# Optimization experiments

Hardware: AMD Instinct MI355X
Metric: run time of the kernel (lower is better)

Reference implementation:

```python
import jax, jax.numpy as jnp
import numpy as np

N, K, F, W = 32768, 32, 4, 256

def setup_inputs() -> dict:
    key = jax.random.key(0)
    ks = jax.random.split(key, 12)
    init = lambda k, shape, fan_in: jax.random.normal(k, shape, jnp.float32) / np.sqrt(fan_in)
    return {
        "h_center": jax.random.normal(ks[0], (N, W), jnp.float32),
        "h_neighbors": jax.random.normal(ks[1], (N, K, W), jnp.float32),
        "differences": jax.random.normal(ks[2], (N, K, F), jnp.float32),
        # filter MLP (depth=2): Dense(W) -> silu -> Dense(W)
        "W_f1": init(ks[3], (F, W), F),
        "b_f1": jnp.zeros((W,), jnp.float32),
        "W_f2": init(ks[4], (W, W), W),
        "b_f2": jnp.zeros((W,), jnp.float32),
        # neighbor projection Dense(W)
        "W_nb": init(ks[5], (W, W), W),
        "b_nb": jnp.zeros((W,), jnp.float32),
        # center projection Dense(W)
        "W_c": init(ks[6], (W, W), W),
        "b_c": jnp.zeros((W,), jnp.float32),
    }

def reference(h_center, h_neighbors, differences, W_f1, b_f1, W_f2, b_f2, W_nb, b_nb, W_c, b_c):
    # filter MLP over edge (difference) features: [N,K,F] -> [N,K,W]
    f = jax.nn.silu(differences @ W_f1 + b_f1)
    filter_kernel = f @ W_f2 + b_f2
    # project neighbor features: [N,K,W]
    h_nb = h_neighbors @ W_nb + b_nb
    # gated message, sum over neighbor axis -> [N,W]
    msg = jnp.sum(filter_kernel * h_nb, axis=-2)
    # center dense + message, silu
    h_out = jax.nn.silu(h_center @ W_c + b_c + msg)
    return h_out
```

## Files before the change

### kernel.cpp

```cpp
#include <hip/hip_runtime.h>
#include <hip/hip_bf16.h>
#include <stdint.h>

#define NN 32768
#define KNBR 32

typedef __attribute__((ext_vector_type(8))) short short8;
typedef __attribute__((ext_vector_type(4))) float f32x4;

__device__ __forceinline__ unsigned int f2bf(float x) {
    union { float f; unsigned int u; } c; c.f = x;
    return (c.u + 0x7FFFu + ((c.u >> 16) & 1u)) >> 16;
}
__device__ __forceinline__ unsigned int pk2(float a, float b) {
    return f2bf(a) | (f2bf(b) << 16);
}
__device__ __forceinline__ unsigned int pkr(float a, float b) {
    unsigned ua = __float_as_uint(a) + 0x8000u;
    unsigned ub = __float_as_uint(b) + 0x8000u;
    return (ua >> 16) | (ub & 0xFFFF0000u);
}
__device__ __forceinline__ float bflo(unsigned u) { return __uint_as_float(u << 16); }
__device__ __forceinline__ float bfhi(unsigned u) { return __uint_as_float(u & 0xFFFF0000u); }
__device__ __forceinline__ float silu_f(float x) {
    return x / (1.0f + __expf(-x));
}

__global__ void prep_weights(const float* __restrict__ Wf2,
                             const float* __restrict__ Wnb,
                             const float* __restrict__ Wc,
                             uint4* __restrict__ ws_out) {
    int t = blockIdx.x * 256 + threadIdx.x;
    int w = t >> 13;
    int q = t & 8191;
    int kt = q >> 10;
    int nt = (q >> 6) & 15;
    int lane = q & 63;
    int k0 = kt * 32 + ((lane >> 4) << 3);
    int col = nt * 16 + (lane & 15);
    const float* src = (w == 0) ? Wf2 : (w == 1) ? Wnb : Wc;
    const float* p = src + (size_t)k0 * 256 + col;
    uint4 o;
    o.x = pk2(p[0],        p[256]);
    o.y = pk2(p[512],      p[768]);
    o.z = pk2(p[1024],     p[1280]);
    o.w = pk2(p[1536],     p[1792]);
    ws_out[t] = o;
}

__global__ __launch_bounds__(1024, 4) void msg_kernel(
        const float* __restrict__ nbr,
        const float* __restrict__ diff,
        const float* __restrict__ Wf1,
        const float* __restrict__ b1,
        const float* __restrict__ b2,
        const float* __restrict__ bnb,
        const uint4* __restrict__ wf2_g,
        const uint4* __restrict__ wnb_g,
        float* __restrict__ msg_out)
{
    __shared__ uint4 w2l[4096];
    __shared__ uint4 wnl[4096];
    __shared__ uint4 fbuf[512];
    __shared__ uint4 ebuf[512];
    __shared__ unsigned w1p[640];

    const int tid  = threadIdx.x;
    const int lane = tid & 63;
    const int wid  = tid >> 6;
    const int wm   = wid >> 2;
    const int wn   = wid & 3;
    const int xcd  = blockIdx.x & 7;
    const int yy   = blockIdx.x >> 3;
    const int chalf = yy & 1;
    const int rgrp  = xcd * 32 + (yy >> 1);
    const size_t rowbase = (size_t)rgrp * 4096;
    const int colbase = chalf * 128;

    const int srow = tid >> 3;
    const int kq4  = (tid & 7) * 4;
    const int kq2  = (tid & 7) * 2;
    unsigned long long* const fdst = (unsigned long long*)
        ((char*)&fbuf[(srow >> 4) * 64 + (kq4 >> 3) * 16 + (srow & 15)] + ((kq4 >> 2) & 1) * 8);
    unsigned long long* const edst = (unsigned long long*)
        ((char*)&ebuf[(srow >> 4) * 64 + (kq4 >> 3) * 16 + (srow & 15)] + ((kq4 >> 2) & 1) * 8);

    auto eload = [&](int g) -> float4 {
        return *(const float4*)(nbr + (rowbase + (size_t)(g >> 3) * 128 + srow) * 256
                                + (g & 7) * 32 + kq4);
    };
    auto dload = [&](int tt) -> float4 {
        return *(const float4*)(diff + (rowbase + (size_t)tt * 128 + srow) * 4);
    };
    auto ewrite = [&](float4 v) {
        unsigned lo = pkr(v.x, v.y), hi = pkr(v.z, v.w);
        *edst = ((unsigned long long)hi << 32) | lo;
    };
    auto fstage = [&](int ktn, float4 d) {
        unsigned ov[2];
        #pragma unroll
        for (int pp = 0; pp < 2; ++pp) {
            const int ci = ktn * 16 + kq2 + pp;
            unsigned c0 = w1p[ci], c1 = w1p[128 + ci], c2 = w1p[256 + ci],
                     c3 = w1p[384 + ci], cb = w1p[512 + ci];
            float pA = bflo(cb) + d.x * bflo(c0) + d.y * bflo(c1)
                                + d.z * bflo(c2) + d.w * bflo(c3);
            float pB = bfhi(cb) + d.x * bfhi(c0) + d.y * bfhi(c1)
                                + d.z * bfhi(c2) + d.w * bfhi(c3);
            ov[pp] = pkr(silu_f(pA), silu_f(pB));
        }
        *fdst = ((unsigned long long)ov[1] << 32) | ov[0];
    };

    #pragma unroll
    for (int i = 0; i < 4; ++i) {
        int idx = tid + i * 1024;
        int kt = idx >> 9, rem = idx & 511;
        int src = kt * 1024 + chalf * 512 + rem;
        w2l[idx] = wf2_g[src];
        wnl[idx] = wnb_g[src];
    }
    if (tid < 512) {
        int j = tid >> 7, p = tid & 127;
        w1p[tid] = pk2(Wf1[j * 256 + 2 * p], Wf1[j * 256 + 2 * p + 1]);
    } else if (tid < 640) {
        int p = tid - 512;
        w1p[tid] = pk2(b1[2 * p], b1[2 * p + 1]);
    }
    float4 d4 = dload(0);
    float4 Ecur = eload(0);
    float vb2[2], vbn[2];
    #pragma unroll
    for (int n = 0; n < 2; ++n) {
        const int col = colbase + wn * 32 + n * 16 + (lane & 15);
        vb2[n] = b2[col];
        vbn[n] = bnb[col];
    }
    __syncthreads();

    ewrite(Ecur);
    fstage(0, d4);
    float4 Enext = eload(1);
    asm volatile("s_waitcnt lgkmcnt(0)" ::: "memory");
    __builtin_amdgcn_sched_barrier(0);
    __builtin_amdgcn_s_barrier();

    f32x4 accP[2][2], accH[2][2];
    #pragma unroll
    for (int m = 0; m < 2; ++m)
        #pragma unroll
        for (int n = 0; n < 2; ++n) {
            accP[m][n] = (f32x4){0.f, 0.f, 0.f, 0.f};
            accH[m][n] = (f32x4){0.f, 0.f, 0.f, 0.f};
        }

    const short8* fb8 = (const short8*)fbuf;
    const short8* eb8 = (const short8*)ebuf;
    const short8* w28 = (const short8*)w2l;
    const short8* wn8 = (const short8*)wnl;

    for (int t = 0; t < 32; ++t) {
        float4 d4n = d4;
        #pragma unroll
        for (int kt = 0; kt < 8; ++kt) {
            const int g = t * 8 + kt;
            if (kt == 0 && t + 1 < 32) d4n = dload(t + 1);
            float4 Efar = Enext;
            if (g + 2 < 256) Efar = eload(g + 2);
            short8 aF0 = fb8[(wm * 2 + 0) * 64 + lane];
            short8 aF1 = fb8[(wm * 2 + 1) * 64 + lane];
            short8 aE0 = eb8[(wm * 2 + 0) * 64 + lane];
            short8 aE1 = eb8[(wm * 2 + 1) * 64 + lane];
            asm volatile("s_waitcnt lgkmcnt(0)" ::: "memory");
            __builtin_amdgcn_sched_barrier(0);
            __builtin_amdgcn_s_barrier();
            short8 B20 = w28[(kt * 8 + wn * 2 + 0) * 64 + lane];
            short8 B21 = w28[(kt * 8 + wn * 2 + 1) * 64 + lane];
            short8 Bn0 = wn8[(kt * 8 + wn * 2 + 0) * 64 + lane];
            short8 Bn1 = wn8[(kt * 8 + wn * 2 + 1) * 64 + lane];
            accP[0][0] = __builtin_amdgcn_mfma_f32_16x16x32_bf16(aF0, B20, accP[0][0], 0, 0, 0);
            accP[0][1] = __builtin_amdgcn_mfma_f32_16x16x32_bf16(aF0, B21, accP[0][1], 0, 0, 0);
            accP[1][0] = __builtin_amdgcn_mfma_f32_16x16x32_bf16(aF1, B20, accP[1][0], 0, 0, 0);
            accP[1][1] = __builtin_amdgcn_mfma_f32_16x16x32_bf16(aF1, B21, accP[1][1], 0, 0, 0);
            accH[0][0] = __builtin_amdgcn_mfma_f32_16x16x32_bf16(aE0, Bn0, accH[0][0], 0, 0, 0);
            accH[0][1] = __builtin_amdgcn_mfma_f32_16x16x32_bf16(aE0, Bn1, accH[0][1], 0, 0, 0);
            accH[1][0] = __builtin_amdgcn_mfma_f32_16x16x32_bf16(aE1, Bn0, accH[1][0], 0, 0, 0);
            accH[1][1] = __builtin_amdgcn_mfma_f32_16x16x32_bf16(aE1, Bn1, accH[1][1], 0, 0, 0);
            if (g + 1 < 256) {
                ewrite(Enext);
                fstage((kt + 1) & 7, (kt == 7) ? d4n : d4);
            }
            if (kt == 7) {
                const size_t node = (size_t)rgrp * 128 + t * 4 + wm;
                #pragma unroll
                for (int n = 0; n < 2; ++n) {
                    float s = 0.f;
                    #pragma unroll
                    for (int m = 0; m < 2; ++m)
                        #pragma unroll
                        for (int r = 0; r < 4; ++r)
                            s += (accP[m][n][r] + vb2[n]) * (accH[m][n][r] + vbn[n]);
                    s += __shfl_xor(s, 16);
                    s += __shfl_xor(s, 32);
                    if (lane < 16)
                        msg_out[node * 256 + colbase + wn * 32 + n * 16 + lane] = s;
                }
                #pragma unroll
                for (int m = 0; m < 2; ++m)
                    #pragma unroll
                    for (int n = 0; n < 2; ++n) {
                        accP[m][n] = (f32x4){0.f, 0.f, 0.f, 0.f};
                        accH[m][n] = (f32x4){0.f, 0.f, 0.f, 0.f};
                    }
            }
            asm volatile("s_waitcnt lgkmcnt(0)" ::: "memory");
            __builtin_amdgcn_sched_barrier(0);
            __builtin_amdgcn_s_barrier();
            Enext = Efar;
        }
        d4 = d4n;
    }
}

__global__ __launch_bounds__(256) void out_kernel(
        const float* __restrict__ hc,
        const float* __restrict__ bc,
        const uint4* __restrict__ wc_g,
        float* __restrict__ out)
{
    __shared__ unsigned short a_s[4 * 2 * 64 * 8];
    __shared__ unsigned short wc_s[2 * 16 * 64 * 8];

    const int tid  = threadIdx.x;
    const int lane = tid & 63;
    const int wn   = tid >> 6;
    const int rblk = blockIdx.x * 64;

    f32x4 acc[4][4];
    #pragma unroll
    for (int mt = 0; mt < 4; ++mt)
        #pragma unroll
        for (int nt = 0; nt < 4; ++nt)
            acc[mt][nt] = (f32x4){0.f, 0.f, 0.f, 0.f};

    uint4* af4 = (uint4*)a_s;
    for (int kt2 = 0; kt2 < 4; ++kt2) {
        {
            int row = tid >> 2, quarter = tid & 3;
            const float* src = hc + (size_t)(rblk + row) * 256 + kt2 * 64 + quarter * 16;
            float4 v0 = *(const float4*)(src + 0);
            float4 v1 = *(const float4*)(src + 4);
            float4 v2 = *(const float4*)(src + 8);
            float4 v3 = *(const float4*)(src + 12);
            uint4 p0, p1;
            p0.x = pk2(v0.x, v0.y); p0.y = pk2(v0.z, v0.w);
            p0.z = pk2(v1.x, v1.y); p0.w = pk2(v1.z, v1.w);
            p1.x = pk2(v2.x, v2.y); p1.y = pk2(v2.z, v2.w);
            p1.z = pk2(v3.x, v3.y); p1.w = pk2(v3.z, v3.w);
            int mt = row >> 4, kti = quarter >> 1, fr = row & 15;
            int g0 = (quarter & 1) * 2;
            af4[(mt * 2 + kti) * 64 + g0 * 16 + fr]       = p0;
            af4[(mt * 2 + kti) * 64 + (g0 + 1) * 16 + fr] = p1;
            const uint4* srcw = wc_g + kt2 * 2048;
            uint4* dw = (uint4*)wc_s;
            #pragma unroll
            for (int j = 0; j < 8; ++j)
                dw[j * 256 + tid] = srcw[j * 256 + tid];
        }
        __syncthreads();
        #pragma unroll
        for (int kti = 0; kti < 2; ++kti) {
            short8 b[4];
            #pragma unroll
            for (int nt = 0; nt < 4; ++nt)
                b[nt] = *(const short8*)&wc_s[((kti * 16 + wn * 4 + nt) * 64 + lane) * 8];
            #pragma unroll
            for (int mt = 0; mt < 4; ++mt) {
                short8 a = *(const short8*)&a_s[((mt * 2 + kti) * 64 + lane) * 8];
                #pragma unroll
                for (int nt = 0; nt < 4; ++nt)
                    acc[mt][nt] = __builtin_amdgcn_mfma_f32_16x16x32_bf16(a, b[nt], acc[mt][nt], 0, 0, 0);
            }
        }
        __syncthreads();
    }

    #pragma unroll
    for (int mt = 0; mt < 4; ++mt)
        #pragma unroll
        for (int nt = 0; nt < 4; ++nt)
            #pragma unroll
            for (int r = 0; r < 4; ++r) {
                int grow = rblk + mt * 16 + ((lane >> 4) << 2) + r;
                int col  = wn * 64 + nt * 16 + (lane & 15);
                size_t idx = (size_t)grow * 256 + col;
                float v = acc[mt][nt][r] + bc[col] + out[idx];
                out[idx] = silu_f(v);
            }
}

extern "C" void kernel_launch(void* const* d_in, const int* in_sizes, int n_in,
                              void* d_out, int out_size, void* d_ws, size_t ws_size,
                              hipStream_t stream) {
    const float* h_center    = (const float*)d_in[0];
    const float* h_neighbors = (const float*)d_in[1];
    const float* differences = (const float*)d_in[2];
    const float* W_f1        = (const float*)d_in[3];
    const float* b_f1        = (const float*)d_in[4];
    const float* W_f2        = (const float*)d_in[5];
    const float* b_f2        = (const float*)d_in[6];
    const float* W_nb        = (const float*)d_in[7];
    const float* b_nb        = (const float*)d_in[8];
    const float* W_c         = (const float*)d_in[9];
    const float* b_c         = (const float*)d_in[10];
    float* out = (float*)d_out;

    uint4* ws4 = (uint4*)d_ws;
    const uint4* wf2_ws = ws4;
    const uint4* wnb_ws = ws4 + 8192;
    const uint4* wc_ws  = ws4 + 16384;

    prep_weights<<<96, 256, 0, stream>>>(W_f2, W_nb, W_c, ws4);
    msg_kernel<<<512, 1024, 0, stream>>>(
        h_neighbors, differences, W_f1, b_f1, b_f2, b_nb, wf2_ws, wnb_ws, out);
    out_kernel<<<NN / 64, 256, 0, stream>>>(h_center, b_c, wc_ws, out);
}
```

Measured before the change: 726.9 us.

## Specialize staging threads for filter and neighbor tiles with swizzled LDS layout

Splits the staging work so the upper 512 threads load and convert neighbor rows as 16-byte chunks, while groups of 128 lower threads each own one k-slice of the filter MLP. Those groups keep their Wf1 and bias coefficients in fp32 registers, which removes the LDS table and its bf16 unpacking. The filter and neighbor buffers now use an XOR-swizzled layout with 16-byte stores, and MFMA fragment reads use a matching permuted lane index, to cut bank conflicts. The cost is load imbalance: the filter work now lands on one 128-thread group per step, and register pressure rises under the 1024-thread launch bound.

```diff
diff --git a/kernel.cpp b/kernel.cpp
--- a/kernel.cpp
+++ b/kernel.cpp
@@ -20,8 +20,6 @@
     unsigned ub = __float_as_uint(b) + 0x8000u;
     return (ua >> 16) | (ub & 0xFFFF0000u);
 }
-__device__ __forceinline__ float bflo(unsigned u) { return __uint_as_float(u << 16); }
-__device__ __forceinline__ float bfhi(unsigned u) { return __uint_as_float(u & 0xFFFF0000u); }
 __device__ __forceinline__ float silu_f(float x) {
     return x / (1.0f + __expf(-x));
 }
@@ -63,7 +61,6 @@
     __shared__ uint4 wnl[4096];
     __shared__ uint4 fbuf[512];
     __shared__ uint4 ebuf[512];
-    __shared__ unsigned w1p[640];
 
     const int tid  = threadIdx.x;
     const int lane = tid & 63;
@@ -77,39 +74,79 @@
     const size_t rowbase = (size_t)rgrp * 4096;
     const int colbase = chalf * 128;
 
-    const int srow = tid >> 3;
-    const int kq4  = (tid & 7) * 4;
-    const int kq2  = (tid & 7) * 2;
-    unsigned long long* const fdst = (unsigned long long*)
-        ((char*)&fbuf[(srow >> 4) * 64 + (kq4 >> 3) * 16 + (srow & 15)] + ((kq4 >> 2) & 1) * 8);
-    unsigned long long* const edst = (unsigned long long*)
-        ((char*)&ebuf[(srow >> 4) * 64 + (kq4 >> 3) * 16 + (srow & 15)] + ((kq4 >> 2) & 1) * 8);
-
-    auto eload = [&](int g) -> float4 {
-        return *(const float4*)(nbr + (rowbase + (size_t)(g >> 3) * 128 + srow) * 256
-                                + (g & 7) * 32 + kq4);
+    const int fo   = tid >> 5;
+    const int fcoh = tid >> 7;
+    const int foq  = fo & 3;
+    const int frr  = tid & 31;
+    const int fidx0 = ((frr >> 4) * 64) + foq * 16 + ((frr & 15) ^ (foq << 2));
+
+    const bool isE = (tid >= 512);
+    const int et   = tid & 511;
+    const int erow = et >> 2, eq = et & 3;
+    const int eidx = ((erow >> 4) * 64) + eq * 16 + ((erow & 15) ^ (eq << 2));
+
+    const int lx = lane ^ ((lane >> 4) << 2);
+
+    float cw[4][8], cb[8];
+    {
+        const int kb = fo * 8;
+        #pragma unroll
+        for (int j = 0; j < 4; ++j) {
+            float4 a = *(const float4*)(Wf1 + j * 256 + kb);
+            float4 b = *(const float4*)(Wf1 + j * 256 + kb + 4);
+            cw[j][0]=a.x; cw[j][1]=a.y; cw[j][2]=a.z; cw[j][3]=a.w;
+            cw[j][4]=b.x; cw[j][5]=b.y; cw[j][6]=b.z; cw[j][7]=b.w;
+        }
+        float4 a = *(const float4*)(b1 + kb);
+        float4 b = *(const float4*)(b1 + kb + 4);
+        cb[0]=a.x; cb[1]=a.y; cb[2]=a.z; cb[3]=a.w;
+        cb[4]=b.x; cb[5]=b.y; cb[6]=b.z; cb[7]=b.w;
+    }
+    float vb2[2], vbn[2];
+    #pragma unroll
+    for (int n = 0; n < 2; ++n) {
+        const int col = colbase + wn * 32 + n * 16 + (lane & 15);
+        vb2[n] = b2[col];
+        vbn[n] = bnb[col];
+    }
+
+    float4 d4r[4];
+    float4 EnA, EnB, EfA, EfB;
+
+    auto dissue = [&](int s) {
+        const size_t rb = rowbase + (size_t)(s >> 3) * 128;
+        #pragma unroll
+        for (int m = 0; m < 4; ++m)
+            d4r[m] = *(const float4*)(diff + (rb + frr + 32 * m) * 4);
     };
-    auto dload = [&](int tt) -> float4 {
-        return *(const float4*)(diff + (rowbase + (size_t)tt * 128 + srow) * 4);
+    auto fstage = [&]() {
+        #pragma unroll
+        for (int m = 0; m < 4; ++m) {
+            const float4 d = d4r[m];
+            unsigned ov[4];
+            #pragma unroll
+            for (int p = 0; p < 4; ++p) {
+                float pA = cb[2*p]   + d.x*cw[0][2*p]   + d.y*cw[1][2*p]
+                                     + d.z*cw[2][2*p]   + d.w*cw[3][2*p];
+                float pB = cb[2*p+1] + d.x*cw[0][2*p+1] + d.y*cw[1][2*p+1]
+                                     + d.z*cw[2][2*p+1] + d.w*cw[3][2*p+1];
+                ov[p] = pkr(silu_f(pA), silu_f(pB));
+            }
+            uint4 o4; o4.x = ov[0]; o4.y = ov[1]; o4.z = ov[2]; o4.w = ov[3];
+            fbuf[fidx0 + m * 128] = o4;
+        }
     };
-    auto ewrite = [&](float4 v) {
-        unsigned lo = pkr(v.x, v.y), hi = pkr(v.z, v.w);
-        *edst = ((unsigned long long)hi << 32) | lo;
+    auto eload = [&](int s, float4& ea, float4& eb) {
+        const float* p = nbr + (rowbase + (size_t)(s >> 3) * 128 + erow) * 256
+                         + (s & 7) * 32 + eq * 8;
+        ea = *(const float4*)p;
+        eb = *(const float4*)(p + 4);
     };
-    auto fstage = [&](int ktn, float4 d) {
-        unsigned ov[2];
-        #pragma unroll
-        for (int pp = 0; pp < 2; ++pp) {
-            const int ci = ktn * 16 + kq2 + pp;
-            unsigned c0 = w1p[ci], c1 = w1p[128 + ci], c2 = w1p[256 + ci],
-                     c3 = w1p[384 + ci], cb = w1p[512 + ci];
-            float pA = bflo(cb) + d.x * bflo(c0) + d.y * bflo(c1)
-                                + d.z * bflo(c2) + d.w * bflo(c3);
-            float pB = bfhi(cb) + d.x * bfhi(c0) + d.y * bfhi(c1)
-                                + d.z * bfhi(c2) + d.w * bfhi(c3);
-            ov[pp] = pkr(silu_f(pA), silu_f(pB));
-        }
-        *fdst = ((unsigned long long)ov[1] << 32) | ov[0];
+    auto ewrite = [&](const float4& ea, const float4& eb) {
+        uint4 o;
+        o.x = pkr(ea.x, ea.y); o.y = pkr(ea.z, ea.w);
+        o.z = pkr(eb.x, eb.y); o.w = pkr(eb.z, eb.w);
+        ebuf[eidx] = o;
     };
 
     #pragma unroll
@@ -120,30 +157,11 @@
         w2l[idx] = wf2_g[src];
         wnl[idx] = wnb_g[src];
     }
-    if (tid < 512) {
-        int j = tid >> 7, p = tid & 127;
-        w1p[tid] = pk2(Wf1[j * 256 + 2 * p], Wf1[j * 256 + 2 * p + 1]);
-    } else if (tid < 640) {
-        int p = tid - 512;
-        w1p[tid] = pk2(b1[2 * p], b1[2 * p + 1]);
-    }
-    float4 d4 = dload(0);
-    float4 Ecur = eload(0);
-    float vb2[2], vbn[2];
-    #pragma unroll
-    for (int n = 0; n < 2; ++n) {
-        const int col = colbase + wn * 32 + n * 16 + (lane & 15);
-        vb2[n] = b2[col];
-        vbn[n] = bnb[col];
-    }
+    if (isE) { float4 a, b; eload(0, a, b); ewrite(a, b); }
+    if (fcoh == 0) { dissue(0); fstage(); }
     __syncthreads();
-
-    ewrite(Ecur);
-    fstage(0, d4);
-    float4 Enext = eload(1);
-    asm volatile("s_waitcnt lgkmcnt(0)" ::: "memory");
-    __builtin_amdgcn_sched_barrier(0);
-    __builtin_amdgcn_s_barrier();
+    if (isE) eload(1, EnA, EnB);
+    if (fcoh == 1) dissue(1);
 
     f32x4 accP[2][2], accH[2][2];
     #pragma unroll
@@ -160,17 +178,19 @@
     const short8* wn8 = (const short8*)wnl;
 
     for (int t = 0; t < 32; ++t) {
-        float4 d4n = d4;
         #pragma unroll
         for (int kt = 0; kt < 8; ++kt) {
             const int g = t * 8 + kt;
-            if (kt == 0 && t + 1 < 32) d4n = dload(t + 1);
-            float4 Efar = Enext;
-            if (g + 2 < 256) Efar = eload(g + 2);
-            short8 aF0 = fb8[(wm * 2 + 0) * 64 + lane];
-            short8 aF1 = fb8[(wm * 2 + 1) * 64 + lane];
-            short8 aE0 = eb8[(wm * 2 + 0) * 64 + lane];
-            short8 aE1 = eb8[(wm * 2 + 1) * 64 + lane];
+            if (g + 2 < 256) {
+                if (isE) eload(g + 2, EfA, EfB);
+                if (((kt + 2) & 7) == fcoh && (g + 2) >> 3 == (g + 2) / 8)
+                    ;
+                if (((g + 2) & 7) == fcoh) dissue(g + 2);
+            }
+            short8 aF0 = fb8[(wm * 2 + 0) * 64 + lx];
+            short8 aF1 = fb8[(wm * 2 + 1) * 64 + lx];
+            short8 aE0 = eb8[(wm * 2 + 0) * 64 + lx];
+            short8 aE1 = eb8[(wm * 2 + 1) * 64 + lx];
             asm volatile("s_waitcnt lgkmcnt(0)" ::: "memory");
             __builtin_amdgcn_sched_barrier(0);
             __builtin_amdgcn_s_barrier();
@@ -187,8 +207,8 @@
             accH[1][0] = __builtin_amdgcn_mfma_f32_16x16x32_bf16(aE1, Bn0, accH[1][0], 0, 0, 0);
             accH[1][1] = __builtin_amdgcn_mfma_f32_16x16x32_bf16(aE1, Bn1, accH[1][1], 0, 0, 0);
             if (g + 1 < 256) {
-                ewrite(Enext);
-                fstage((kt + 1) & 7, (kt == 7) ? d4n : d4);
+                if (isE) ewrite(EnA, EnB);
+                if (((g + 1) & 7) == fcoh) fstage();
             }
             if (kt == 7) {
                 const size_t node = (size_t)rgrp * 128 + t * 4 + wm;
@@ -216,9 +236,8 @@
             asm volatile("s_waitcnt lgkmcnt(0)" ::: "memory");
             __builtin_amdgcn_sched_barrier(0);
             __builtin_amdgcn_s_barrier();
-            Enext = Efar;
-        }
-        d4 = d4n;
+            EnA = EfA; EnB = EfB;
+        }
     }
 }
 
```

New measurement: 1.748 ms. +140.5%, slower.

## Precompute filter-MLP first layer into global bf16 fragments; double-buffer neighbor tile

Applied to the files above, without the earlier changes.

Moves silu(differences@W_f1+b_f1) out of the main message kernel into a separate prep_f kernel. That kernel writes the result as bf16 MFMA A-fragments to workspace, and msg_kernel reads them directly from global with one step of register prefetch. The neighbor LDS buffer becomes double-buffered, which removes one of the two block barriers per k-step. The intent is to take the per-step VALU/exp work and a barrier off the MFMA loop. In exchange it adds roughly a 512MB intermediate that is written once and read by both column halves, and it relies on the workspace being large enough.

```diff
diff --git a/kernel.cpp b/kernel.cpp
--- a/kernel.cpp
+++ b/kernel.cpp
@@ -20,8 +20,6 @@
     unsigned ub = __float_as_uint(b) + 0x8000u;
     return (ua >> 16) | (ub & 0xFFFF0000u);
 }
-__device__ __forceinline__ float bflo(unsigned u) { return __uint_as_float(u << 16); }
-__device__ __forceinline__ float bfhi(unsigned u) { return __uint_as_float(u & 0xFFFF0000u); }
 __device__ __forceinline__ float silu_f(float x) {
     return x / (1.0f + __expf(-x));
 }
@@ -48,22 +46,64 @@
     ws_out[t] = o;
 }
 
-__global__ __launch_bounds__(1024, 4) void msg_kernel(
-        const float* __restrict__ nbr,
+__global__ __launch_bounds__(256) void prep_f(
         const float* __restrict__ diff,
         const float* __restrict__ Wf1,
         const float* __restrict__ b1,
+        uint4* __restrict__ fout)
+{
+    const int bid  = blockIdx.x;
+    const int kt   = bid & 7;
+    const size_t g128 = (size_t)(bid >> 3);
+    const int tid  = threadIdx.x;
+    const int lane = tid & 63;
+    const int wv   = tid >> 6;
+    const int kgrp = lane >> 4, r16 = lane & 15;
+    const int k0   = kt * 32 + kgrp * 8;
+
+    float4 cwa[4], cwb[4];
+    #pragma unroll
+    for (int j = 0; j < 4; ++j) {
+        cwa[j] = *(const float4*)(Wf1 + j * 256 + k0);
+        cwb[j] = *(const float4*)(Wf1 + j * 256 + k0 + 4);
+    }
+    const float4 cba = *(const float4*)(b1 + k0);
+    const float4 cbb = *(const float4*)(b1 + k0 + 4);
+
+    #pragma unroll
+    for (int mi = 0; mi < 2; ++mi) {
+        const int mt = mi * 4 + wv;
+        const size_t row = g128 * 128 + mt * 16 + r16;
+        const float4 d = *(const float4*)(diff + row * 4);
+        float v0 = cba.x + d.x*cwa[0].x + d.y*cwa[1].x + d.z*cwa[2].x + d.w*cwa[3].x;
+        float v1 = cba.y + d.x*cwa[0].y + d.y*cwa[1].y + d.z*cwa[2].y + d.w*cwa[3].y;
+        float v2 = cba.z + d.x*cwa[0].z + d.y*cwa[1].z + d.z*cwa[2].z + d.w*cwa[3].z;
+        float v3 = cba.w + d.x*cwa[0].w + d.y*cwa[1].w + d.z*cwa[2].w + d.w*cwa[3].w;
+        float v4 = cbb.x + d.x*cwb[0].x + d.y*cwb[1].x + d.z*cwb[2].x + d.w*cwb[3].x;
+        float v5 = cbb.y + d.x*cwb[0].y + d.y*cwb[1].y + d.z*cwb[2].y + d.w*cwb[3].y;
+        float v6 = cbb.z + d.x*cwb[0].z + d.y*cwb[1].z + d.z*cwb[2].z + d.w*cwb[3].z;
+        float v7 = cbb.w + d.x*cwb[0].w + d.y*cwb[1].w + d.z*cwb[2].w + d.w*cwb[3].w;
+        uint4 o;
+        o.x = pkr(silu_f(v0), silu_f(v1));
+        o.y = pkr(silu_f(v2), silu_f(v3));
+        o.z = pkr(silu_f(v4), silu_f(v5));
+        o.w = pkr(silu_f(v6), silu_f(v7));
+        fout[(size_t)bid * 512 + mt * 64 + lane] = o;
+    }
+}
+
+__global__ __launch_bounds__(1024, 4) void msg_kernel(
+        const float* __restrict__ nbr,
         const float* __restrict__ b2,
         const float* __restrict__ bnb,
         const uint4* __restrict__ wf2_g,
         const uint4* __restrict__ wnb_g,
+        const uint4* __restrict__ ffrag,
         float* __restrict__ msg_out)
 {
     __shared__ uint4 w2l[4096];
     __shared__ uint4 wnl[4096];
-    __shared__ uint4 fbuf[512];
-    __shared__ uint4 ebuf[512];
-    __shared__ unsigned w1p[640];
+    __shared__ uint4 ebuf[2][512];
 
     const int tid  = threadIdx.x;
     const int lane = tid & 63;
@@ -77,39 +117,27 @@
     const size_t rowbase = (size_t)rgrp * 4096;
     const int colbase = chalf * 128;
 
-    const int srow = tid >> 3;
-    const int kq4  = (tid & 7) * 4;
-    const int kq2  = (tid & 7) * 2;
-    unsigned long long* const fdst = (unsigned long long*)
-        ((char*)&fbuf[(srow >> 4) * 64 + (kq4 >> 3) * 16 + (srow & 15)] + ((kq4 >> 2) & 1) * 8);
-    unsigned long long* const edst = (unsigned long long*)
-        ((char*)&ebuf[(srow >> 4) * 64 + (kq4 >> 3) * 16 + (srow & 15)] + ((kq4 >> 2) & 1) * 8);
+    const int s    = tid >> 1;
+    const int half = tid & 1;
+    const int emt  = s >> 6;
+    const int ekg  = (s >> 4) & 3;
+    const int erow = s & 15;
 
     auto eload = [&](int g) -> float4 {
-        return *(const float4*)(nbr + (rowbase + (size_t)(g >> 3) * 128 + srow) * 256
-                                + (g & 7) * 32 + kq4);
+        const int t = g >> 3, kt = g & 7;
+        return *(const float4*)(nbr + (rowbase + (size_t)t * 128 + emt * 16 + erow) * 256
+                                + kt * 32 + ekg * 8 + half * 4);
     };
-    auto dload = [&](int tt) -> float4 {
-        return *(const float4*)(diff + (rowbase + (size_t)tt * 128 + srow) * 4);
+    auto ewrite = [&](int pb, const float4& v) {
+        unsigned lo = pkr(v.x, v.y), hi = pkr(v.z, v.w);
+        *(unsigned long long*)((char*)&ebuf[pb][s] + half * 8) =
+            ((unsigned long long)hi << 32) | lo;
     };
-    auto ewrite = [&](float4 v) {
-        unsigned lo = pkr(v.x, v.y), hi = pkr(v.z, v.w);
-        *edst = ((unsigned long long)hi << 32) | lo;
-    };
-    auto fstage = [&](int ktn, float4 d) {
-        unsigned ov[2];
-        #pragma unroll
-        for (int pp = 0; pp < 2; ++pp) {
-            const int ci = ktn * 16 + kq2 + pp;
-            unsigned c0 = w1p[ci], c1 = w1p[128 + ci], c2 = w1p[256 + ci],
-                     c3 = w1p[384 + ci], cb = w1p[512 + ci];
-            float pA = bflo(cb) + d.x * bflo(c0) + d.y * bflo(c1)
-                                + d.z * bflo(c2) + d.w * bflo(c3);
-            float pB = bfhi(cb) + d.x * bfhi(c0) + d.y * bfhi(c1)
-                                + d.z * bfhi(c2) + d.w * bfhi(c3);
-            ov[pp] = pkr(silu_f(pA), silu_f(pB));
-        }
-        *fdst = ((unsigned long long)ov[1] << 32) | ov[0];
+    const short8* fbase = (const short8*)ffrag;
+    auto fload = [&](int g, short8& a0, short8& a1) {
+        const size_t fb = ((size_t)(rgrp * 32 + (g >> 3)) * 8 + (g & 7)) * 512;
+        a0 = fbase[fb + (wm * 2 + 0) * 64 + lane];
+        a1 = fbase[fb + (wm * 2 + 1) * 64 + lane];
     };
 
     #pragma unroll
@@ -120,15 +148,6 @@
         w2l[idx] = wf2_g[src];
         wnl[idx] = wnb_g[src];
     }
-    if (tid < 512) {
-        int j = tid >> 7, p = tid & 127;
-        w1p[tid] = pk2(Wf1[j * 256 + 2 * p], Wf1[j * 256 + 2 * p + 1]);
-    } else if (tid < 640) {
-        int p = tid - 512;
-        w1p[tid] = pk2(b1[2 * p], b1[2 * p + 1]);
-    }
-    float4 d4 = dload(0);
-    float4 Ecur = eload(0);
     float vb2[2], vbn[2];
     #pragma unroll
     for (int n = 0; n < 2; ++n) {
@@ -136,14 +155,11 @@
         vb2[n] = b2[col];
         vbn[n] = bnb[col];
     }
+    ewrite(0, eload(0));
+    float4 EnA = eload(1);
+    short8 aF0c, aF1c;
+    fload(0, aF0c, aF1c);
     __syncthreads();
-
-    ewrite(Ecur);
-    fstage(0, d4);
-    float4 Enext = eload(1);
-    asm volatile("s_waitcnt lgkmcnt(0)" ::: "memory");
-    __builtin_amdgcn_sched_barrier(0);
-    __builtin_amdgcn_s_barrier();
 
     f32x4 accP[2][2], accH[2][2];
     #pragma unroll
@@ -154,56 +170,48 @@
             accH[m][n] = (f32x4){0.f, 0.f, 0.f, 0.f};
         }
 
-    const short8* fb8 = (const short8*)fbuf;
-    const short8* eb8 = (const short8*)ebuf;
     const short8* w28 = (const short8*)w2l;
     const short8* wn8 = (const short8*)wnl;
 
     for (int t = 0; t < 32; ++t) {
-        float4 d4n = d4;
         #pragma unroll
         for (int kt = 0; kt < 8; ++kt) {
             const int g = t * 8 + kt;
-            if (kt == 0 && t + 1 < 32) d4n = dload(t + 1);
-            float4 Efar = Enext;
-            if (g + 2 < 256) Efar = eload(g + 2);
-            short8 aF0 = fb8[(wm * 2 + 0) * 64 + lane];
-            short8 aF1 = fb8[(wm * 2 + 1) * 64 + lane];
+            const int pb = g & 1;
+            float4 EfA;
+            if (g + 2 < 256) EfA = eload(g + 2);
+            short8 aF0n, aF1n;
+            if (g + 1 < 256) fload(g + 1, aF0n, aF1n);
+            const short8* eb8 = (const short8*)ebuf[pb];
             short8 aE0 = eb8[(wm * 2 + 0) * 64 + lane];
             short8 aE1 = eb8[(wm * 2 + 1) * 64 + lane];
-            asm volatile("s_waitcnt lgkmcnt(0)" ::: "memory");
-            __builtin_amdgcn_sched_barrier(0);
-            __builtin_amdgcn_s_barrier();
             short8 B20 = w28[(kt * 8 + wn * 2 + 0) * 64 + lane];
             short8 B21 = w28[(kt * 8 + wn * 2 + 1) * 64 + lane];
             short8 Bn0 = wn8[(kt * 8 + wn * 2 + 0) * 64 + lane];
             short8 Bn1 = wn8[(kt * 8 + wn * 2 + 1) * 64 + lane];
-            accP[0][0] = __builtin_amdgcn_mfma_f32_16x16x32_bf16(aF0, B20, accP[0][0], 0, 0, 0);
-            accP[0][1] = __builtin_amdgcn_mfma_f32_16x16x32_bf16(aF0, B21, accP[0][1], 0, 0, 0);
-            accP[1][0] = __builtin_amdgcn_mfma_f32_16x16x32_bf16(aF1, B20, accP[1][0], 0, 0, 0);
-            accP[1][1] = __builtin_amdgcn_mfma_f32_16x16x32_bf16(aF1, B21, accP[1][1], 0, 0, 0);
+            accP[0][0] = __builtin_amdgcn_mfma_f32_16x16x32_bf16(aF0c, B20, accP[0][0], 0, 0, 0);
+            accP[0][1] = __builtin_amdgcn_mfma_f32_16x16x32_bf16(aF0c, B21, accP[0][1], 0, 0, 0);
+            accP[1][0] = __builtin_amdgcn_mfma_f32_16x16x32_bf16(aF1c, B20, accP[1][0], 0, 0, 0);
+            accP[1][1] = __builtin_amdgcn_mfma_f32_16x16x32_bf16(aF1c, B21, accP[1][1], 0, 0, 0);
             accH[0][0] = __builtin_amdgcn_mfma_f32_16x16x32_bf16(aE0, Bn0, accH[0][0], 0, 0, 0);
             accH[0][1] = __builtin_amdgcn_mfma_f32_16x16x32_bf16(aE0, Bn1, accH[0][1], 0, 0, 0);
             accH[1][0] = __builtin_amdgcn_mfma_f32_16x16x32_bf16(aE1, Bn0, accH[1][0], 0, 0, 0);
             accH[1][1] = __builtin_amdgcn_mfma_f32_16x16x32_bf16(aE1, Bn1, accH[1][1], 0, 0, 0);
-            if (g + 1 < 256) {
-                ewrite(Enext);
-                fstage((kt + 1) & 7, (kt == 7) ? d4n : d4);
-            }
+            if (g + 1 < 256) ewrite(pb ^ 1, EnA);
             if (kt == 7) {
                 const size_t node = (size_t)rgrp * 128 + t * 4 + wm;
                 #pragma unroll
                 for (int n = 0; n < 2; ++n) {
-                    float s = 0.f;
+                    float sv = 0.f;
                     #pragma unroll
                     for (int m = 0; m < 2; ++m)
                         #pragma unroll
                         for (int r = 0; r < 4; ++r)
-                            s += (accP[m][n][r] + vb2[n]) * (accH[m][n][r] + vbn[n]);
-                    s += __shfl_xor(s, 16);
-                    s += __shfl_xor(s, 32);
+                            sv += (accP[m][n][r] + vb2[n]) * (accH[m][n][r] + vbn[n]);
+                    sv += __shfl_xor(sv, 16);
+                    sv += __shfl_xor(sv, 32);
                     if (lane < 16)
-                        msg_out[node * 256 + colbase + wn * 32 + n * 16 + lane] = s;
+                        msg_out[node * 256 + colbase + wn * 32 + n * 16 + lane] = sv;
                 }
                 #pragma unroll
                 for (int m = 0; m < 2; ++m)
@@ -216,9 +224,9 @@
             asm volatile("s_waitcnt lgkmcnt(0)" ::: "memory");
             __builtin_amdgcn_sched_barrier(0);
             __builtin_amdgcn_s_barrier();
-            Enext = Efar;
+            EnA = EfA;
+            aF0c = aF0n; aF1c = aF1n;
         }
-        d4 = d4n;
     }
 }
 
@@ -319,9 +327,11 @@
     const uint4* wf2_ws = ws4;
     const uint4* wnb_ws = ws4 + 8192;
     const uint4* wc_ws  = ws4 + 16384;
+    uint4* f_ws         = ws4 + 24576;
 
     prep_weights<<<96, 256, 0, stream>>>(W_f2, W_nb, W_c, ws4);
+    prep_f<<<65536, 256, 0, stream>>>(differences, W_f1, b_f1, f_ws);
     msg_kernel<<<512, 1024, 0, stream>>>(
-        h_neighbors, differences, W_f1, b_f1, b_f2, b_nb, wf2_ws, wnb_ws, out);
+        h_neighbors, b_f2, b_nb, wf2_ws, wnb_ws, f_ws, out);
     out_kernel<<<NN / 64, 256, 0, stream>>>(h_center, b_c, wc_ws, out);
 }
```

Result: faster. 709.9 us (-2.3%).
